# Optimization experiments

Hardware: AMD Instinct MI355X
Metric: run time of the kernel (lower is better)

The kernel has to match this reference:

```python
import jax, jax.numpy as jnp
import numpy as np

CMIN, CMAX = -1024.0, 1016.0  # clamp(min=-2**10, max=2**10 - 8) after every op
BRIGHT_F = 1.9   # 1.0 + linspace(0, 0.9, 11)[10]
COLOR_F = 1.9    # 1.0 + linspace(0, 0.9, 11)[10]


def _brightness_dct(x, f):
    # pixel-domain multiplicative brightness; DCT is linear -> scale all coeffs
    return x * f


def _contrast_dct(x, f):
    # pixel contrast: (p - mean)*f + mean.
    # In DCT: AC coeffs scale by f; DC coeff blends toward per-channel mean DC.
    dc_mean = jnp.mean(x[..., 0, 0], axis=(-2, -1), keepdims=True)  # [C,1,1]
    out = x * f
    out = out.at[..., 0, 0].add((1.0 - f) * dc_mean)
    return out


def setup_inputs() -> dict:
    key = jax.random.key(0)
    k1, k2 = jax.random.split(key)
    # luma: [C=1, Hblocks, Wblocks, 8, 8]; chroma 4:2:0: [C=2, H/2, W/2, 8, 8]
    y = jax.random.normal(k1, (1, 512, 512, 8, 8), dtype=jnp.float32) * 100.0
    c = jax.random.normal(k2, (2, 256, 256, 8, 8), dtype=jnp.float32) * 100.0
    return {"y": y, "c": c}


def reference(y, c):
    clamp = lambda t: jnp.clip(t, CMIN, CMAX)
    # dct_prep(mode='start') treated as identity; initial clamp as in forward()
    y = clamp(y)
    c = clamp(c)
    # op 1: Brightness on luma (coeff[0]); both planes clamped after each op
    y = clamp(_brightness_dct(y, BRIGHT_F))
    c = clamp(c)
    # op 2: Color = contrast on chroma (coeff[1])
    c = clamp(_contrast_dct(c, COLOR_F))
    y = clamp(y)
    # dct_prep(mode='end') treated as identity
    return y, c
```

## Files before the change

kernel.cpp:

```cpp
#include <hip/hip_runtime.h>

#define CMIN -1024.0f
#define CMAX 1016.0f

__device__ __forceinline__ float clampv(float x) {
    return fminf(fmaxf(x, CMIN), CMAX);
}

__global__ void __launch_bounds__(256)
dc_sum_kernel(const float* __restrict__ c, float* __restrict__ ws,
              int dc_per_ch) {
    int t = blockIdx.x * blockDim.x + threadIdx.x;
    float v = clampv(c[(size_t)t * 64]);

    #pragma unroll
    for (int off = 32; off > 0; off >>= 1)
        v += __shfl_down(v, off, 64);

    __shared__ float smem[4];
    int lane = threadIdx.x & 63;
    int wave = threadIdx.x >> 6;
    if (lane == 0) smem[wave] = v;
    __syncthreads();
    if (threadIdx.x == 0) {
        float s = smem[0] + smem[1] + smem[2] + smem[3];
        int ch = (blockIdx.x * 256 < dc_per_ch) ? 0 : 1;
        atomicAdd(&ws[ch], s);
    }
}

__global__ void __launch_bounds__(256)
fused_elementwise(const float4* __restrict__ y, const float4* __restrict__ c,
                  float4* __restrict__ out, const float* __restrict__ ws,
                  int ynvec, int total_nvec, int c_half_nvec,
                  float inv_count) {
    int i = blockIdx.x * blockDim.x + threadIdx.x;
    if (i >= total_nvec) return;

    if (i < ynvec) {
        float4 v = y[i];
        v.x = clampv(clampv(v.x) * 1.9f);
        v.y = clampv(clampv(v.y) * 1.9f);
        v.z = clampv(clampv(v.z) * 1.9f);
        v.w = clampv(clampv(v.w) * 1.9f);
        out[i] = v;
    } else {
        int ci = i - ynvec;
        float4 v = c[ci];
        float4 r;
        r.x = clampv(v.x) * 1.9f;
        r.y = clampv(v.y) * 1.9f;
        r.z = clampv(v.z) * 1.9f;
        r.w = clampv(v.w) * 1.9f;
        if ((ci & 15) == 0) {
            int ch = (ci < c_half_nvec) ? 0 : 1;
            r.x += -0.9f * (ws[ch] * inv_count);
        }
        r.x = clampv(r.x);
        r.y = clampv(r.y);
        r.z = clampv(r.z);
        r.w = clampv(r.w);
        out[i] = r;
    }
}

extern "C" void kernel_launch(void* const* d_in, const int* in_sizes, int n_in,
                              void* d_out, int out_size, void* d_ws, size_t ws_size,
                              hipStream_t stream) {
    const float* y = (const float*)d_in[0];
    const float* c = (const float*)d_in[1];
    float* out = (float*)d_out;

    const int yN = in_sizes[0];
    const int cN = in_sizes[1];

    float* ws = (float*)d_ws;

    hipMemsetAsync(ws, 0, 2 * sizeof(float), stream);

    const int dc_count = cN / 64;
    const int dc_per_ch = dc_count / 2;
    dc_sum_kernel<<<dc_count / 256, 256, 0, stream>>>(c, ws, dc_per_ch);

    const int ynvec = yN / 4;
    const int cnvec = cN / 4;
    const int total_nvec = ynvec + cnvec;
    const float inv_count = 1.0f / (float)dc_per_ch;
    fused_elementwise<<<(total_nvec + 255) / 256, 256, 0, stream>>>(
        (const float4*)y, (const float4*)c, (float4*)out, ws,
        ynvec, total_nvec, cnvec / 2, inv_count);
}
```

Baseline: 184.2 us.

## Fuse DC reduction and elementwise pass into one cooperative grid-synced kernel

Replaces the memset, DC-sum kernel and elementwise kernel with a single cooperative kernel of 1024 blocks. Each block computes partial DC sums while processing the luma plane, writes per-block partials, and after a grid-wide sync every block reduces the partials and processes chroma with the mean adjustment. This removes two launches, the memset and the atomics, and overlaps the DC reads with luma streaming. In exchange it adds a grid barrier and a fixed persistent grid size, and it hardcodes the 512 partial-sum layout to the input shapes.

```diff
diff --git a/kernel.cpp b/kernel.cpp
--- a/kernel.cpp
+++ b/kernel.cpp
@@ -1,4 +1,7 @@
 #include <hip/hip_runtime.h>
+#include <hip/hip_cooperative_groups.h>
+
+namespace cg = cooperative_groups;
 
 #define CMIN -1024.0f
 #define CMAX 1016.0f
@@ -7,60 +10,72 @@
     return fminf(fmaxf(x, CMIN), CMAX);
 }
 
-__global__ void __launch_bounds__(256)
-dc_sum_kernel(const float* __restrict__ c, float* __restrict__ ws,
-              int dc_per_ch) {
-    int t = blockIdx.x * blockDim.x + threadIdx.x;
-    float v = clampv(c[(size_t)t * 64]);
-
+__device__ __forceinline__ float wave_reduce(float v) {
     #pragma unroll
     for (int off = 32; off > 0; off >>= 1)
         v += __shfl_down(v, off, 64);
-
-    __shared__ float smem[4];
-    int lane = threadIdx.x & 63;
-    int wave = threadIdx.x >> 6;
-    if (lane == 0) smem[wave] = v;
-    __syncthreads();
-    if (threadIdx.x == 0) {
-        float s = smem[0] + smem[1] + smem[2] + smem[3];
-        int ch = (blockIdx.x * 256 < dc_per_ch) ? 0 : 1;
-        atomicAdd(&ws[ch], s);
-    }
+    return v;
 }
 
 __global__ void __launch_bounds__(256)
-fused_elementwise(const float4* __restrict__ y, const float4* __restrict__ c,
-                  float4* __restrict__ out, const float* __restrict__ ws,
-                  int ynvec, int total_nvec, int c_half_nvec,
-                  float inv_count) {
-    int i = blockIdx.x * blockDim.x + threadIdx.x;
-    if (i >= total_nvec) return;
+fused_all(const float4* __restrict__ y4, const float* __restrict__ c,
+          const float4* __restrict__ c4, float4* __restrict__ out,
+          float* __restrict__ ws, int ynvec, int cnvec, int c_half_nvec,
+          int dc_count, float neg09_inv_count)
+{
+    const int tid = blockIdx.x * blockDim.x + threadIdx.x;
+    const int T   = gridDim.x * blockDim.x;
+    const int lane = threadIdx.x & 63;
+    const int wave = threadIdx.x >> 6;
+    __shared__ float smem[8];
 
-    if (i < ynvec) {
-        float4 v = y[i];
+    float dcv = 0.0f;
+    if (tid < dc_count) dcv = clampv(c[(size_t)tid * 64]);
+
+    for (int i = tid; i < ynvec; i += T) {
+        float4 v = y4[i];
         v.x = clampv(clampv(v.x) * 1.9f);
         v.y = clampv(clampv(v.y) * 1.9f);
         v.z = clampv(clampv(v.z) * 1.9f);
         v.w = clampv(clampv(v.w) * 1.9f);
         out[i] = v;
-    } else {
-        int ci = i - ynvec;
-        float4 v = c[ci];
+    }
+
+    float s = wave_reduce(dcv);
+    if (lane == 0) smem[wave] = s;
+    __syncthreads();
+    if (threadIdx.x == 0)
+        ws[blockIdx.x] = smem[0] + smem[1] + smem[2] + smem[3];
+
+    cg::this_grid().sync();
+
+    float p0 = wave_reduce(ws[threadIdx.x]);
+    float p1 = wave_reduce(ws[256 + threadIdx.x]);
+    if (lane == 0) { smem[wave] = p0; smem[4 + wave] = p1; }
+    __syncthreads();
+    if (threadIdx.x == 0) {
+        smem[0] = (smem[0] + smem[1] + smem[2] + smem[3]) * neg09_inv_count;
+        smem[4] = (smem[4] + smem[5] + smem[6] + smem[7]) * neg09_inv_count;
+    }
+    __syncthreads();
+    const float adj0 = smem[0];
+    const float adj1 = smem[4];
+
+    float4* outc = out + ynvec;
+    for (int i = tid; i < cnvec; i += T) {
+        float4 v = c4[i];
         float4 r;
         r.x = clampv(v.x) * 1.9f;
         r.y = clampv(v.y) * 1.9f;
         r.z = clampv(v.z) * 1.9f;
         r.w = clampv(v.w) * 1.9f;
-        if ((ci & 15) == 0) {
-            int ch = (ci < c_half_nvec) ? 0 : 1;
-            r.x += -0.9f * (ws[ch] * inv_count);
-        }
+        if ((i & 15) == 0)
+            r.x += (i < c_half_nvec) ? adj0 : adj1;
         r.x = clampv(r.x);
         r.y = clampv(r.y);
         r.z = clampv(r.z);
         r.w = clampv(r.w);
-        out[i] = r;
+        outc[i] = r;
     }
 }
 
@@ -70,23 +85,25 @@
     const float* y = (const float*)d_in[0];
     const float* c = (const float*)d_in[1];
     float* out = (float*)d_out;
+    float* ws  = (float*)d_ws;
 
     const int yN = in_sizes[0];
     const int cN = in_sizes[1];
 
-    float* ws = (float*)d_ws;
+    int ynvec       = yN / 4;
+    int cnvec       = cN / 4;
+    int c_half_nvec = cnvec / 2;
+    int dc_count    = cN / 64;
+    float neg09_inv_count = -0.9f / (float)(dc_count / 2);
 
-    hipMemsetAsync(ws, 0, 2 * sizeof(float), stream);
+    const float4* y4 = (const float4*)y;
+    const float4* c4 = (const float4*)c;
 
-    const int dc_count = cN / 64;
-    const int dc_per_ch = dc_count / 2;
-    dc_sum_kernel<<<dc_count / 256, 256, 0, stream>>>(c, ws, dc_per_ch);
+    void* args[] = {(void*)&y4, (void*)&c, (void*)&c4, (void*)&out,
+                    (void*)&ws, (void*)&ynvec, (void*)&cnvec,
+                    (void*)&c_half_nvec, (void*)&dc_count,
+                    (void*)&neg09_inv_count};
 
-    const int ynvec = yN / 4;
-    const int cnvec = cN / 4;
-    const int total_nvec = ynvec + cnvec;
-    const float inv_count = 1.0f / (float)dc_per_ch;
-    fused_elementwise<<<(total_nvec + 255) / 256, 256, 0, stream>>>(
-        (const float4*)y, (const float4*)c, (float4*)out, ws,
-        ynvec, total_nvec, cnvec / 2, inv_count);
+    hipLaunchCooperativeKernel((void*)fused_all, dim3(1024), dim3(256),
+                               args, 0, stream);
 }
```

New measurement: 281.1 us. 1.53x slower.
